# Kernel optimization log

Measured on AMD Instinct MI355X. Metric: run time of the kernel, lower is better.

The kernel has to match this reference:

```python
import jax, jax.numpy as jnp
import numpy as np
from jax import lax

VOCAB, EMBED_DIM, NUM_TAGS = 50000, 300, 16
BATCH, SEQ = 64, 512


def setup_inputs() -> dict:
    key = jax.random.key(0)
    k0, k1, k2, k3, k4 = jax.random.split(key, 5)
    text = jax.random.randint(k0, (BATCH, SEQ), 0, VOCAB)
    tags = jax.random.randint(k1, (BATCH, SEQ), 0, NUM_TAGS)
    embed_table = jax.random.normal(k2, (VOCAB, EMBED_DIM), jnp.float32) * 0.02
    W = jax.random.normal(k3, (EMBED_DIM, NUM_TAGS), jnp.float32) * 0.05
    b = jnp.zeros((NUM_TAGS,), jnp.float32)
    trans = jax.random.uniform(k4, (NUM_TAGS, NUM_TAGS), jnp.float32)
    return {"text": text, "tags": tags, "embed_table": embed_table, "W": W, "b": b, "trans": trans}


def crf_log_likelihood(probs, tags, lens, trans):
    # probs: [B,S,T] unary potentials; tags: [B,S] int; lens: [B]; trans: [T,T]
    B, S, T = probs.shape
    t_idx = jnp.arange(S)
    mask = (t_idx[None, :] < lens[:, None])  # [B,S] valid positions

    # --- gold sequence score ---
    unary = jnp.take_along_axis(probs, tags[..., None], axis=2)[..., 0]  # [B,S]
    unary_score = jnp.sum(unary * mask, axis=1)
    btrans = trans[tags[:, :-1], tags[:, 1:]]            # [B,S-1]
    bmask = mask[:, 1:]                                   # transition t->t+1 valid iff t+1 < len
    binary_score = jnp.sum(btrans * bmask, axis=1)

    # --- forward algorithm (log partition) ---
    alpha0 = probs[:, 0]                                  # [B,T]
    emits = jnp.moveaxis(probs[:, 1:], 0, 1)              # [S-1,B,T]
    ms = jnp.moveaxis(mask[:, 1:], 0, 1)                  # [S-1,B]

    def step(alpha, inp):
        emit, m = inp
        new = jax.nn.logsumexp(alpha[:, :, None] + trans[None, :, :], axis=1) + emit
        return jnp.where(m[:, None], new, alpha), None

    alpha, _ = lax.scan(step, alpha0, (emits, ms))
    log_norm = jax.nn.logsumexp(alpha, axis=-1)           # [B]
    return unary_score + binary_score - log_norm


def reference(text, tags, embed_table, W, b, trans):
    # dropout is identity in eval/reference mode
    text_lens = jnp.sum((text != 0).astype(jnp.int32), axis=1)  # [B]
    probs = embed_table[text] @ W + b                            # [B,S,T]
    log_likelihood = crf_log_likelihood(probs, tags, text_lens, trans)
    return probs, text_lens, log_likelihood
```

## Files before the change

kernel.cpp:

```cpp
#include <hip/hip_runtime.h>
#include <hip/hip_bf16.h>

#define VOCAB 50000
#define ED    300
#define NT    16
#define BB    64
#define SS    512

#define LOG2E 1.4426950408889634f
#define LN2   0.6931471805599453f
#define WSTR  308

__global__ __launch_bounds__(256) void probs_kernel(const int* __restrict__ text,
                                                    const float* __restrict__ emb,
                                                    const float* __restrict__ W,
                                                    const float* __restrict__ bias,
                                                    float* __restrict__ out_probs) {
  __shared__ float wt[NT * WSTR];

  const int tid = threadIdx.x;
  const int lane = tid & 63, wave = tid >> 6;
  const int r = lane >> 4, t = lane & 15;
  const int row = blockIdx.x * 16 + wave * 4 + r;

  for (int e = tid; e < ED * NT; e += 256) {
    int d = e >> 4, tt = e & 15;
    wt[tt * WSTR + d] = W[e];
  }

  const int tok = text[row];
  const float4* erow = (const float4*)(emb + (size_t)tok * ED);
  float acc = bias[t];

  float4 A[8];
#pragma unroll
  for (int i = 0; i < 8; ++i) A[i] = erow[i];

  __syncthreads();

  const float4* w4 = (const float4*)(wt + t * WSTR);
#pragma unroll
  for (int c = 0; c < 75; ++c) {
    float4 e = A[c & 7];
    if (c < 67) A[c & 7] = erow[c + 8];
    float4 w = w4[c];
    acc = fmaf(e.x, w.x, acc);
    acc = fmaf(e.y, w.y, acc);
    acc = fmaf(e.z, w.z, acc);
    acc = fmaf(e.w, w.w, acc);
  }
  out_probs[(size_t)row * NT + t] = acc;
}

template <int CTRL>
__device__ __forceinline__ float dppmov(float x) {
  int xi = __float_as_int(x);
  return __int_as_float(
      __builtin_amdgcn_update_dpp(xi, xi, CTRL, 0xF, 0xF, false));
}

__device__ __forceinline__ float crf_step(float g, float pe, const float E[16]) {
  float gn, h, m, c, a1, a2, a3;
  asm("s_nop 1\n\t"
      "v_mov_b32_dpp %[h], %[g] row_half_mirror row_mask:0xf bank_mask:0xf\n\t"
      "v_mov_b32_dpp %[m], %[g] row_mirror row_mask:0xf bank_mask:0xf\n\t"
      "v_mul_f32 %[gn], %[g], %[e0]\n\t"
      "v_fmac_f32_dpp %[gn], %[g], %[e1] quad_perm:[1,0,3,2] row_mask:0xf bank_mask:0xf\n\t"
      "v_fmac_f32_dpp %[gn], %[g], %[e2] quad_perm:[2,3,0,1] row_mask:0xf bank_mask:0xf\n\t"
      "v_fmac_f32_dpp %[gn], %[g], %[e3] quad_perm:[3,2,1,0] row_mask:0xf bank_mask:0xf\n\t"
      "v_mov_b32_dpp %[c], %[m] row_half_mirror row_mask:0xf bank_mask:0xf\n\t"
      "v_mul_f32 %[a1], %[h], %[e7]\n\t"
      "v_fmac_f32_dpp %[a1], %[h], %[e6] quad_perm:[1,0,3,2] row_mask:0xf bank_mask:0xf\n\t"
      "v_fmac_f32_dpp %[a1], %[h], %[e5] quad_perm:[2,3,0,1] row_mask:0xf bank_mask:0xf\n\t"
      "v_fmac_f32_dpp %[a1], %[h], %[e4] quad_perm:[3,2,1,0] row_mask:0xf bank_mask:0xf\n\t"
      "v_mul_f32 %[a2], %[m], %[e15]\n\t"
      "v_fmac_f32_dpp %[a2], %[m], %[e14] quad_perm:[1,0,3,2] row_mask:0xf bank_mask:0xf\n\t"
      "v_fmac_f32_dpp %[a2], %[m], %[e13] quad_perm:[2,3,0,1] row_mask:0xf bank_mask:0xf\n\t"
      "v_fmac_f32_dpp %[a2], %[m], %[e12] quad_perm:[3,2,1,0] row_mask:0xf bank_mask:0xf\n\t"
      "v_mul_f32 %[a3], %[c], %[e8]\n\t"
      "v_fmac_f32_dpp %[a3], %[c], %[e9] quad_perm:[1,0,3,2] row_mask:0xf bank_mask:0xf\n\t"
      "v_fmac_f32_dpp %[a3], %[c], %[e10] quad_perm:[2,3,0,1] row_mask:0xf bank_mask:0xf\n\t"
      "v_fmac_f32_dpp %[a3], %[c], %[e11] quad_perm:[3,2,1,0] row_mask:0xf bank_mask:0xf\n\t"
      "v_add_f32 %[gn], %[gn], %[a1]\n\t"
      "v_add_f32 %[a2], %[a2], %[a3]\n\t"
      "v_add_f32 %[gn], %[gn], %[a2]\n\t"
      "v_mul_f32 %[gn], %[gn], %[pe]"
      : [gn] "=&v"(gn), [h] "=&v"(h), [m] "=&v"(m), [c] "=&v"(c),
        [a1] "=&v"(a1), [a2] "=&v"(a2), [a3] "=&v"(a3)
      : [g] "v"(g), [pe] "v"(pe),
        [e0] "v"(E[0]), [e1] "v"(E[1]), [e2] "v"(E[2]), [e3] "v"(E[3]),
        [e4] "v"(E[4]), [e5] "v"(E[5]), [e6] "v"(E[6]), [e7] "v"(E[7]),
        [e8] "v"(E[8]), [e9] "v"(E[9]), [e10] "v"(E[10]), [e11] "v"(E[11]),
        [e12] "v"(E[12]), [e13] "v"(E[13]), [e14] "v"(E[14]), [e15] "v"(E[15]));
  return gn;
}

__global__ __launch_bounds__(64) void crf_kernel(const int* __restrict__ text,
                                                 const int* __restrict__ tags,
                                                 const float* __restrict__ trans,
                                                 const float* __restrict__ probs,
                                                 float* __restrict__ out_lens,
                                                 float* __restrict__ out_ll) {
  __shared__ float lps[(SS + 1) * NT];
  __shared__ int tgs[SS];
  __shared__ float trs[256];

  const int tid = threadIdx.x;
  const int j = tid & 15;
  const int b = blockIdx.x;

  {
    const float4* p4 = (const float4*)(probs + (size_t)b * SS * NT);
    float4* l4 = (float4*)lps;
#pragma unroll
    for (int i = 0; i < 32; ++i) {
      float4 v = p4[tid + 64 * i];
      v.x *= LOG2E; v.y *= LOG2E; v.z *= LOG2E; v.w *= LOG2E;
      l4[tid + 64 * i] = v;
    }
    const int4* t4 = (const int4*)(tags + b * SS);
    int4* lt = (int4*)tgs;
#pragma unroll
    for (int i = 0; i < 2; ++i) lt[tid + 64 * i] = t4[tid + 64 * i];
    for (int i = tid; i < 256; i += 64) trs[i] = trans[i];
  }
  __syncthreads();

  const int* tx = text + b * SS;
  int cnt = 0;
#pragma unroll
  for (int k = 0; k < 8; ++k) cnt += (tx[tid + 64 * k] != 0) ? 1 : 0;
  for (int off = 32; off > 0; off >>= 1) cnt += __shfl_xor(cnt, off, 64);
  const int len = cnt;
  if (tid == 0) out_lens[b] = (float)len;

  float su = 0.f, sb = 0.f;
#pragma unroll
  for (int it = 0; it < 8; ++it) {
    const int s = tid + 64 * it;
    if (s < len) {
      int t1 = tgs[s];
      su += lps[s * NT + t1];
      if (s >= 1) sb += trs[tgs[s - 1] * 16 + t1];
    }
  }
  float sc = fmaf(su, LN2, sb);
  for (int off = 32; off > 0; off >>= 1) sc += __shfl_xor(sc, off, 64);

  float E[16];
#pragma unroll
  for (int k = 0; k < 16; ++k) E[k] = __expf(trs[((j ^ k) << 4) + j]) * 0.03125f;

  float g = exp2f(lps[j]);
  float K2 = 0.f;

  const int T = (len > 0) ? len - 1 : 0;
  const int nfull = T >> 4;
  const int rem = T & 15;

  float raw[16];
#pragma unroll
  for (int c = 0; c < 16; ++c) raw[c] = lps[(1 + c) * NT + j];

  int s0 = 1;
  for (int blk = 0; blk < nfull; ++blk) {
#pragma unroll
    for (int c = 0; c < 16; ++c) {
      float pe = exp2f(raw[c]);
      raw[c] = lps[(s0 + 16 + c) * NT + j];
      g = crf_step(g, pe, E);
    }
    if ((blk & 3) == 3) {
      float mx = g;
      mx = fmaxf(mx, dppmov<0xB1>(mx));
      mx = fmaxf(mx, dppmov<0x4E>(mx));
      mx = fmaxf(mx, dppmov<0x141>(mx));
      mx = fmaxf(mx, dppmov<0x140>(mx));
      float rr = 1.0f / mx;
      K2 -= __log2f(rr);
      g *= rr;
    }
    s0 += 16;
  }
  for (int c = 0; c < rem; ++c) {
    float pe = exp2f(raw[c]);
    g = crf_step(g, pe, E);
  }

  float x = g;
  x += dppmov<0xB1>(x);
  x += dppmov<0x4E>(x);
  x += dppmov<0x141>(x);
  x += dppmov<0x140>(x);
  float log_norm = LN2 * (K2 + 5.0f * (float)T + __log2f(x));
  if (tid == 0) out_ll[b] = sc - log_norm;
}

extern "C" void kernel_launch(void* const* d_in, const int* in_sizes, int n_in,
                              void* d_out, int out_size, void* d_ws, size_t ws_size,
                              hipStream_t stream) {
  const int* text = (const int*)d_in[0];
  const int* tags = (const int*)d_in[1];
  const float* emb = (const float*)d_in[2];
  const float* W = (const float*)d_in[3];
  const float* bias = (const float*)d_in[4];
  const float* trans = (const float*)d_in[5];

  float* out = (float*)d_out;
  float* out_probs = out;
  float* out_lens = out + BB * SS * NT;
  float* out_ll = out + BB * SS * NT + BB;

  probs_kernel<<<(BB * SS) / 16, 256, 0, stream>>>(text, emb, W, bias, out_probs);
  crf_kernel<<<BB, 64, 0, stream>>>(text, tags, trans, out_probs, out_lens, out_ll);
}
```

Baseline: 151.2 us.

## Parallelize CRF forward recursion across sequence chunks via transfer-matrix products

```diff
diff --git a/kernel.cpp b/kernel.cpp
--- a/kernel.cpp
+++ b/kernel.cpp
@@ -59,118 +59,140 @@
       __builtin_amdgcn_update_dpp(xi, xi, CTRL, 0xF, 0xF, false));
 }
 
-__device__ __forceinline__ float crf_step(float g, float pe, const float E[16]) {
-  float gn, h, m, c, a1, a2, a3;
-  asm("s_nop 1\n\t"
-      "v_mov_b32_dpp %[h], %[g] row_half_mirror row_mask:0xf bank_mask:0xf\n\t"
-      "v_mov_b32_dpp %[m], %[g] row_mirror row_mask:0xf bank_mask:0xf\n\t"
-      "v_mul_f32 %[gn], %[g], %[e0]\n\t"
-      "v_fmac_f32_dpp %[gn], %[g], %[e1] quad_perm:[1,0,3,2] row_mask:0xf bank_mask:0xf\n\t"
-      "v_fmac_f32_dpp %[gn], %[g], %[e2] quad_perm:[2,3,0,1] row_mask:0xf bank_mask:0xf\n\t"
-      "v_fmac_f32_dpp %[gn], %[g], %[e3] quad_perm:[3,2,1,0] row_mask:0xf bank_mask:0xf\n\t"
-      "v_mov_b32_dpp %[c], %[m] row_half_mirror row_mask:0xf bank_mask:0xf\n\t"
-      "v_mul_f32 %[a1], %[h], %[e7]\n\t"
-      "v_fmac_f32_dpp %[a1], %[h], %[e6] quad_perm:[1,0,3,2] row_mask:0xf bank_mask:0xf\n\t"
-      "v_fmac_f32_dpp %[a1], %[h], %[e5] quad_perm:[2,3,0,1] row_mask:0xf bank_mask:0xf\n\t"
-      "v_fmac_f32_dpp %[a1], %[h], %[e4] quad_perm:[3,2,1,0] row_mask:0xf bank_mask:0xf\n\t"
-      "v_mul_f32 %[a2], %[m], %[e15]\n\t"
-      "v_fmac_f32_dpp %[a2], %[m], %[e14] quad_perm:[1,0,3,2] row_mask:0xf bank_mask:0xf\n\t"
-      "v_fmac_f32_dpp %[a2], %[m], %[e13] quad_perm:[2,3,0,1] row_mask:0xf bank_mask:0xf\n\t"
-      "v_fmac_f32_dpp %[a2], %[m], %[e12] quad_perm:[3,2,1,0] row_mask:0xf bank_mask:0xf\n\t"
-      "v_mul_f32 %[a3], %[c], %[e8]\n\t"
-      "v_fmac_f32_dpp %[a3], %[c], %[e9] quad_perm:[1,0,3,2] row_mask:0xf bank_mask:0xf\n\t"
-      "v_fmac_f32_dpp %[a3], %[c], %[e10] quad_perm:[2,3,0,1] row_mask:0xf bank_mask:0xf\n\t"
-      "v_fmac_f32_dpp %[a3], %[c], %[e11] quad_perm:[3,2,1,0] row_mask:0xf bank_mask:0xf\n\t"
-      "v_add_f32 %[gn], %[gn], %[a1]\n\t"
-      "v_add_f32 %[a2], %[a2], %[a3]\n\t"
-      "v_add_f32 %[gn], %[gn], %[a2]\n\t"
-      "v_mul_f32 %[gn], %[gn], %[pe]"
-      : [gn] "=&v"(gn), [h] "=&v"(h), [m] "=&v"(m), [c] "=&v"(c),
-        [a1] "=&v"(a1), [a2] "=&v"(a2), [a3] "=&v"(a3)
-      : [g] "v"(g), [pe] "v"(pe),
-        [e0] "v"(E[0]), [e1] "v"(E[1]), [e2] "v"(E[2]), [e3] "v"(E[3]),
-        [e4] "v"(E[4]), [e5] "v"(E[5]), [e6] "v"(E[6]), [e7] "v"(E[7]),
-        [e8] "v"(E[8]), [e9] "v"(E[9]), [e10] "v"(E[10]), [e11] "v"(E[11]),
-        [e12] "v"(E[12]), [e13] "v"(E[13]), [e14] "v"(E[14]), [e15] "v"(E[15]));
-  return gn;
-}
-
-__global__ __launch_bounds__(64) void crf_kernel(const int* __restrict__ text,
-                                                 const int* __restrict__ tags,
-                                                 const float* __restrict__ trans,
-                                                 const float* __restrict__ probs,
-                                                 float* __restrict__ out_lens,
-                                                 float* __restrict__ out_ll) {
-  __shared__ float lps[(SS + 1) * NT];
+__device__ __forceinline__ void allgather16(float g, float lam[16]) {
+  lam[0] = g;
+  lam[1] = dppmov<0xB1>(g);
+  lam[2] = dppmov<0x4E>(g);
+  lam[3] = dppmov<0x1B>(g);
+  float h = dppmov<0x141>(g);
+  lam[7] = h;
+  lam[6] = dppmov<0xB1>(h);
+  lam[5] = dppmov<0x4E>(h);
+  lam[4] = dppmov<0x1B>(h);
+  float m = dppmov<0x140>(g);
+  lam[15] = m;
+  lam[14] = dppmov<0xB1>(m);
+  lam[13] = dppmov<0x4E>(m);
+  lam[12] = dppmov<0x1B>(m);
+  float c = dppmov<0x141>(m);
+  lam[8] = c;
+  lam[9]  = dppmov<0xB1>(c);
+  lam[10] = dppmov<0x4E>(c);
+  lam[11] = dppmov<0x1B>(c);
+}
+
+__device__ __forceinline__ float crf_step_c(float g, float pe, const float E[16]) {
+  float h = dppmov<0x141>(g);
+  float m = dppmov<0x140>(g);
+  float c = dppmov<0x141>(m);
+  float s0 = fmaf(dppmov<0x1B>(g), E[3],
+             fmaf(dppmov<0x4E>(g), E[2], fmaf(dppmov<0xB1>(g), E[1], g * E[0])));
+  float s1 = fmaf(dppmov<0x1B>(h), E[4],
+             fmaf(dppmov<0x4E>(h), E[5], fmaf(dppmov<0xB1>(h), E[6], h * E[7])));
+  float s2 = fmaf(dppmov<0x1B>(m), E[12],
+             fmaf(dppmov<0x4E>(m), E[13], fmaf(dppmov<0xB1>(m), E[14], m * E[15])));
+  float s3 = fmaf(dppmov<0x1B>(c), E[11],
+             fmaf(dppmov<0x4E>(c), E[10], fmaf(dppmov<0xB1>(c), E[9], c * E[8])));
+  return ((s0 + s1) + (s2 + s3)) * pe;
+}
+
+__global__ __launch_bounds__(1024, 4) void crf_kernel(
+    const int* __restrict__ text, const int* __restrict__ tags,
+    const float* __restrict__ trans, const float* __restrict__ probs,
+    float* __restrict__ out_lens, float* __restrict__ out_ll) {
+  __shared__ float lps[SS * NT];
+  __shared__ float pw[16 * 256];
   __shared__ int tgs[SS];
   __shared__ float trs[256];
+  __shared__ float red_su[16], red_sb[16];
+  __shared__ int red_cnt[16];
 
   const int tid = threadIdx.x;
-  const int j = tid & 15;
+  const int wave = tid >> 6, lane = tid & 63;
+  const int j = lane & 15, row16 = (lane >> 4) & 3;
   const int b = blockIdx.x;
 
   {
     const float4* p4 = (const float4*)(probs + (size_t)b * SS * NT);
     float4* l4 = (float4*)lps;
 #pragma unroll
-    for (int i = 0; i < 32; ++i) {
-      float4 v = p4[tid + 64 * i];
+    for (int i = 0; i < 2; ++i) {
+      float4 v = p4[tid + 1024 * i];
       v.x *= LOG2E; v.y *= LOG2E; v.z *= LOG2E; v.w *= LOG2E;
-      l4[tid + 64 * i] = v;
+      l4[tid + 1024 * i] = v;
     }
-    const int4* t4 = (const int4*)(tags + b * SS);
-    int4* lt = (int4*)tgs;
-#pragma unroll
-    for (int i = 0; i < 2; ++i) lt[tid + 64 * i] = t4[tid + 64 * i];
-    for (int i = tid; i < 256; i += 64) trs[i] = trans[i];
-  }
-  __syncthreads();
-
-  const int* tx = text + b * SS;
-  int cnt = 0;
-#pragma unroll
-  for (int k = 0; k < 8; ++k) cnt += (tx[tid + 64 * k] != 0) ? 1 : 0;
-  for (int off = 32; off > 0; off >>= 1) cnt += __shfl_xor(cnt, off, 64);
-  const int len = cnt;
+    if (tid < 128) ((int4*)tgs)[tid] = ((const int4*)(tags + b * SS))[tid];
+    if (tid < 256) trs[tid] = trans[tid];
+  }
+  __syncthreads();
+
+  int cpart = 0;
+  if (tid < SS) cpart = (text[b * SS + tid] != 0) ? 1 : 0;
+  for (int off = 32; off > 0; off >>= 1) cpart += __shfl_xor(cpart, off, 64);
+  if (lane == 0) red_cnt[wave] = cpart;
+  __syncthreads();
+  int len = 0;
+#pragma unroll
+  for (int w = 0; w < 16; ++w) len += red_cnt[w];
   if (tid == 0) out_lens[b] = (float)len;
 
   float su = 0.f, sb = 0.f;
-#pragma unroll
-  for (int it = 0; it < 8; ++it) {
-    const int s = tid + 64 * it;
-    if (s < len) {
-      int t1 = tgs[s];
-      su += lps[s * NT + t1];
-      if (s >= 1) sb += trs[tgs[s - 1] * 16 + t1];
-    }
-  }
-  float sc = fmaf(su, LN2, sb);
-  for (int off = 32; off > 0; off >>= 1) sc += __shfl_xor(sc, off, 64);
+  if (tid < SS && tid < len) {
+    int t1 = tgs[tid];
+    su = lps[tid * NT + t1];
+    if (tid >= 1) sb = trs[tgs[tid - 1] * 16 + t1];
+  }
+  for (int off = 32; off > 0; off >>= 1) su += __shfl_xor(su, off, 64);
+  for (int off = 32; off > 0; off >>= 1) sb += __shfl_xor(sb, off, 64);
+  if (lane == 0) { red_su[wave] = su; red_sb[wave] = sb; }
 
   float E[16];
 #pragma unroll
   for (int k = 0; k < 16; ++k) E[k] = __expf(trs[((j ^ k) << 4) + j]) * 0.03125f;
+
+  const int s_start = 1 + 32 * wave;
+  int nst = len - s_start;
+  nst = (nst < 0) ? 0 : ((nst > 32) ? 32 : nst);
+
+  float p0 = (j == 4 * row16 + 0) ? 1.f : 0.f;
+  float p1 = (j == 4 * row16 + 1) ? 1.f : 0.f;
+  float p2 = (j == 4 * row16 + 2) ? 1.f : 0.f;
+  float p3 = (j == 4 * row16 + 3) ? 1.f : 0.f;
+
+#pragma unroll 4
+  for (int c = 0; c < nst; ++c) {
+    float pe = exp2f(lps[(s_start + c) * NT + j]);
+    p0 = crf_step_c(p0, pe, E);
+    p1 = crf_step_c(p1, pe, E);
+    p2 = crf_step_c(p2, pe, E);
+    p3 = crf_step_c(p3, pe, E);
+  }
+
+  {
+    float* dst = pw + wave * 256;
+    dst[(4 * row16 + 0) * 16 + j] = p0;
+    dst[(4 * row16 + 1) * 16 + j] = p1;
+    dst[(4 * row16 + 2) * 16 + j] = p2;
+    dst[(4 * row16 + 3) * 16 + j] = p3;
+  }
+  __syncthreads();
+
+  if (wave != 0) return;
 
   float g = exp2f(lps[j]);
   float K2 = 0.f;
-
   const int T = (len > 0) ? len - 1 : 0;
-  const int nfull = T >> 4;
-  const int rem = T & 15;
-
-  float raw[16];
-#pragma unroll
-  for (int c = 0; c < 16; ++c) raw[c] = lps[(1 + c) * NT + j];
-
-  int s0 = 1;
-  for (int blk = 0; blk < nfull; ++blk) {
-#pragma unroll
-    for (int c = 0; c < 16; ++c) {
-      float pe = exp2f(raw[c]);
-      raw[c] = lps[(s0 + 16 + c) * NT + j];
-      g = crf_step(g, pe, E);
-    }
-    if ((blk & 3) == 3) {
+
+  for (int w = 0; w < 16; ++w) {
+    int n = len - (1 + 32 * w);
+    if (n > 0) {
+      float lam[16];
+      allgather16(g, lam);
+      const float* A = pw + w * 256;
+      float acc = 0.f;
+#pragma unroll
+      for (int k = 0; k < 16; ++k) acc = fmaf(lam[k], A[((j ^ k) << 4) + j], acc);
+      g = acc;
       float mx = g;
       mx = fmaxf(mx, dppmov<0xB1>(mx));
       mx = fmaxf(mx, dppmov<0x4E>(mx));
@@ -180,11 +202,6 @@
       K2 -= __log2f(rr);
       g *= rr;
     }
-    s0 += 16;
-  }
-  for (int c = 0; c < rem; ++c) {
-    float pe = exp2f(raw[c]);
-    g = crf_step(g, pe, E);
   }
 
   float x = g;
@@ -192,8 +209,14 @@
   x += dppmov<0x4E>(x);
   x += dppmov<0x141>(x);
   x += dppmov<0x140>(x);
+
+  float su_t = 0.f, sb_t = 0.f;
+#pragma unroll
+  for (int w = 0; w < 16; ++w) { su_t += red_su[w]; sb_t += red_sb[w]; }
+  float sc = fmaf(su_t, LN2, sb_t);
+
   float log_norm = LN2 * (K2 + 5.0f * (float)T + __log2f(x));
-  if (tid == 0) out_ll[b] = sc - log_norm;
+  if (lane == 0) out_ll[b] = sc - log_norm;
 }
 
 extern "C" void kernel_launch(void* const* d_in, const int* in_sizes, int n_in,
@@ -212,5 +235,5 @@
   float* out_ll = out + BB * SS * NT + BB;
 
   probs_kernel<<<(BB * SS) / 16, 256, 0, stream>>>(text, emb, W, bias, out_probs);
-  crf_kernel<<<BB, 64, 0, stream>>>(text, tags, trans, out_probs, out_lens, out_ll);
-}
+  crf_kernel<<<BB, 1024, 0, stream>>>(text, tags, trans, out_probs, out_lens, out_ll);
+}
```

Measured after the change: 159.8 us. 1.06x slower.
